# Kernel optimization log

Measured on AMD Instinct MI355X. Metric: run time of the kernel, lower is better.

Reference implementation:

```python
import jax, jax.numpy as jnp
import numpy as np

B, TQ, TV, D, UNITS = 4, 256, 256, 512, 512
NEG_INF = -1e9

def setup_inputs() -> dict:
    key = jax.random.key(0)
    ks = jax.random.split(key, 5)
    return {
        "query": jax.random.normal(ks[0], (B, TQ, D), dtype=jnp.float32),
        "value": jax.random.normal(ks[1], (B, TV, D), dtype=jnp.float32),
        "mask": jnp.ones((B, TV), dtype=bool),
        "W1": jax.random.normal(ks[2], (D, UNITS), dtype=jnp.float32) * (1.0 / np.sqrt(D)),
        "W2": jax.random.normal(ks[3], (D, UNITS), dtype=jnp.float32) * (1.0 / np.sqrt(D)),
        "scale": jax.random.normal(ks[4], (UNITS,), dtype=jnp.float32),
    }

def reference(query, value, mask, W1, W2, scale):
    # Dual projections
    q = query @ W1                      # [B,Tq,U]
    k = value @ W2                      # [B,Tv,U]
    # Additive (Bahdanau) scores: sum(scale * tanh(q + k)) over units
    # broadcast tensor [B,Tq,Tv,U] is what the kernel would tile/fuse away
    t = jnp.tanh(q[:, :, None, :] + k[:, None, :, :])   # [B,Tq,Tv,U]
    scores = jnp.einsum('btvu,u->btv', t, scale)         # [B,Tq,Tv]
    # mask over value (key) positions
    scores = jnp.where(mask[:, None, :], scores, NEG_INF)
    attn = jax.nn.softmax(scores, axis=-1)               # [B,Tq,Tv]
    context = jnp.einsum('btv,bvd->btd', attn, value)    # [B,Tq,D]
    return context, attn
```

## Files before the change

### kernel.cpp

```cpp
#include <hip/hip_runtime.h>

typedef float f4 __attribute__((ext_vector_type(4)));
typedef float f2 __attribute__((ext_vector_type(2)));
typedef short short8 __attribute__((ext_vector_type(8)));
typedef float f32x4 __attribute__((ext_vector_type(4)));

#define NEG_INF -1e9f

__device__ inline void bsplit(float x, unsigned short& h, unsigned short& l) {
  union { float f; unsigned u; } a; a.f = x;
  unsigned rh = (a.u + 0x7fffu + ((a.u >> 16) & 1u)) >> 16;
  h = (unsigned short)rh;
  union { unsigned u; float f; } b; b.u = rh << 16;
  union { float f; unsigned u; } c; c.f = x - b.f;
  unsigned rl = (c.u + 0x7fffu + ((c.u >> 16) & 1u)) >> 16;
  l = (unsigned short)rl;
}

__device__ inline void gl_lds16(const void* g, void* l) {
  __builtin_amdgcn_global_load_lds(
      (const __attribute__((address_space(1))) unsigned int*)g,
      (__attribute__((address_space(3))) unsigned int*)l, 16, 0, 0);
}

__global__ __launch_bounds__(256) void conv_aw(
    const float* __restrict__ q, const float* __restrict__ v,
    const float* __restrict__ W1, const float* __restrict__ W2,
    unsigned short* __restrict__ Ahi, unsigned short* __restrict__ Alo,
    unsigned short* __restrict__ Whi, unsigned short* __restrict__ Wlo)
{
  __shared__ float ldsW[128][64];
  const int t = threadIdx.x;

  if (blockIdx.x < 512) {
    const int g = blockIdx.x * 256 + t;
    const int row64 = g & 63;
    const int panel = (g >> 6) & 31;
    const int kc    = g >> 11;
    const int rowg  = panel * 64 + row64;
    const float* src = (rowg < 1024) ? (q + (size_t)rowg * 512 + kc * 8)
                                     : (v + (size_t)(rowg - 1024) * 512 + kc * 8);
    f4 x0 = *reinterpret_cast<const f4*>(src);
    f4 x1 = *reinterpret_cast<const f4*>(src + 4);
    unsigned short h[8], l[8];
#pragma unroll
    for (int j = 0; j < 4; ++j) { bsplit(x0[j], h[j], l[j]); bsplit(x1[j], h[4+j], l[4+j]); }
    const size_t off = ((size_t)(panel * 64 + kc) * 64 + row64) * 8;
    short8 ph, pl;
#pragma unroll
    for (int j = 0; j < 8; ++j) { ph[j] = (short)h[j]; pl[j] = (short)l[j]; }
    *reinterpret_cast<short8*>(&Ahi[off]) = ph;
    *reinterpret_cast<short8*>(&Alo[off]) = pl;
    return;
  }

  const int bid   = blockIdx.x - 512;
  const int kslab = bid & 3;
  const int np    = (bid >> 2) & 7;
  const int z     = bid >> 5;
  const float* __restrict__ W = z ? W2 : W1;
  const int k0 = kslab * 128, n0 = np * 64;

#pragma unroll
  for (int it = 0; it < 8; ++it) {
    const int idx = it * 256 + t;
    const int kr  = idx >> 4;
    const int nc4 = (idx & 15) * 4;
    *reinterpret_cast<f4*>(&ldsW[kr][nc4]) =
        *reinterpret_cast<const f4*>(&W[(size_t)(k0 + kr) * 512 + n0 + nc4]);
  }
  __syncthreads();

  const int wpanel = z * 8 + np;
  const int n = t & 63;
#pragma unroll
  for (int it = 0; it < 4; ++it) {
    const int kcl = it * 4 + (t >> 6);
    short8 ph, pl;
#pragma unroll
    for (int j = 0; j < 8; ++j) {
      unsigned short h, l;
      bsplit(ldsW[kcl * 8 + j][n], h, l);
      ph[j] = (short)h; pl[j] = (short)l;
    }
    const size_t off = ((size_t)(wpanel * 64 + kslab * 16 + kcl) * 64 + n) * 8;
    *reinterpret_cast<short8*>(&Whi[off]) = ph;
    *reinterpret_cast<short8*>(&Wlo[off]) = pl;
  }
}

__global__ __launch_bounds__(256) void projmm(
    const unsigned short* __restrict__ Ahi, const unsigned short* __restrict__ Alo,
    const unsigned short* __restrict__ Whi, const unsigned short* __restrict__ Wlo,
    float* __restrict__ EQ, float* __restrict__ EKT)
{
  const int nb = blockIdx.x, mb = blockIdx.y, z = blockIdx.z;
  const int t = threadIdx.x;
  const int l = t & 63;
  const int w = t >> 6;
  const int wr = w >> 1, wc = w & 1;

  __shared__ __align__(16) short Ast[2][2][2048];
  __shared__ __align__(16) short Bst[2][2][2048];
  __shared__ float ldsT[64][67];

  const unsigned short* abase_h = Ahi + (size_t)(z * 16 + mb) * 32768;
  const unsigned short* abase_l = Alo + (size_t)(z * 16 + mb) * 32768;
  const unsigned short* wbase_h = Whi + (size_t)(z * 8 + nb) * 32768;
  const unsigned short* wbase_l = Wlo + (size_t)(z * 8 + nb) * 32768;

  const int ldst = (t >> 6) * 512;
  const int gsrc = t * 8;

#define STAGE(buf, ks)                                                        \
  do {                                                                        \
    gl_lds16(abase_h + (ks) * 2048 + gsrc, &Ast[buf][0][ldst]);               \
    gl_lds16(abase_l + (ks) * 2048 + gsrc, &Ast[buf][1][ldst]);               \
    gl_lds16(wbase_h + (ks) * 2048 + gsrc, &Bst[buf][0][ldst]);               \
    gl_lds16(wbase_l + (ks) * 2048 + gsrc, &Bst[buf][1][ldst]);               \
  } while (0)

  f32x4 acc[2][2] = {};
  STAGE(0, 0);
  __syncthreads();

  int buf = 0;
  for (int ks = 0; ks < 16; ++ks) {
    if (ks < 15) STAGE(buf ^ 1, ks + 1);
    const int kgo = (l >> 4) * 1024;
    short8 ah[2], al[2], bh[2], bl[2];
#pragma unroll
    for (int i = 0; i < 2; ++i) {
      const int ro = (wr * 32 + i * 16 + (l & 15)) * 16;
      ah[i] = *reinterpret_cast<const short8*>((const char*)&Ast[buf][0][0] + kgo + ro);
      al[i] = *reinterpret_cast<const short8*>((const char*)&Ast[buf][1][0] + kgo + ro);
    }
#pragma unroll
    for (int j = 0; j < 2; ++j) {
      const int co = (wc * 32 + j * 16 + (l & 15)) * 16;
      bh[j] = *reinterpret_cast<const short8*>((const char*)&Bst[buf][0][0] + kgo + co);
      bl[j] = *reinterpret_cast<const short8*>((const char*)&Bst[buf][1][0] + kgo + co);
    }
#pragma unroll
    for (int i = 0; i < 2; ++i)
#pragma unroll
      for (int j = 0; j < 2; ++j) {
        acc[i][j] = __builtin_amdgcn_mfma_f32_16x16x32_bf16(ah[i], bh[j], acc[i][j], 0, 0, 0);
        acc[i][j] = __builtin_amdgcn_mfma_f32_16x16x32_bf16(ah[i], bl[j], acc[i][j], 0, 0, 0);
        acc[i][j] = __builtin_amdgcn_mfma_f32_16x16x32_bf16(al[i], bh[j], acc[i][j], 0, 0, 0);
      }
    __syncthreads();
    buf ^= 1;
  }

  if (z == 0) {
#pragma unroll
    for (int i = 0; i < 2; ++i)
#pragma unroll
      for (int j = 0; j < 2; ++j)
#pragma unroll
        for (int r = 0; r < 4; ++r) {
          const int row = mb * 64 + wr * 32 + i * 16 + (l >> 4) * 4 + r;
          const int col = nb * 64 + wc * 32 + j * 16 + (l & 15);
          EQ[(size_t)row * 512 + col] = __expf(2.0f * acc[i][j][r]);
        }
  } else {
#pragma unroll
    for (int i = 0; i < 2; ++i)
#pragma unroll
      for (int j = 0; j < 2; ++j)
#pragma unroll
        for (int r = 0; r < 4; ++r) {
          const int rl = wr * 32 + i * 16 + (l >> 4) * 4 + r;
          const int cl = wc * 32 + j * 16 + (l & 15);
          ldsT[rl][cl] = __expf(2.0f * acc[i][j][r]);
        }
    __syncthreads();
    const int b  = (mb * 64) >> 8;
    const int v0 = (mb * 64) & 255;
    const int vl = t & 63;
#pragma unroll
    for (int it = 0; it < 16; ++it) {
      const int ul = it * 4 + (t >> 6);
      EKT[(size_t)b * 131072 + (size_t)(nb * 64 + ul) * 256 + v0 + vl] = ldsT[vl][ul];
    }
  }
#undef STAGE
}

__global__ __launch_bounds__(1024) void bah_attn(
    const float* __restrict__ EQ, const float* __restrict__ EKT,
    const float* __restrict__ value, const int* __restrict__ mask,
    const float* __restrict__ scale,
    float* __restrict__ ctx_out, float* __restrict__ attn_out)
{
  const int blk = blockIdx.x;
  const int b  = (blk & 7) >> 1;
  const int tg = (blk >> 3) + ((blk & 1) << 5);
  const int tq0 = tg * 4;
  const int bq  = b * 256 + tq0;

  const int tid = threadIdx.x;
  const int v4  = tid & 63;
  const int uq  = tid >> 6;
  const int w   = tid >> 6;
  const int l   = tid & 63;

  __shared__ f4    eq4s[512];
  __shared__ float ss[512];
  __shared__ float wredM[4][4];
  __shared__ float wredS[4][4];
  __shared__ float sumS_lds;
  __shared__ float atT[256][4];
  __shared__ __align__(16) char uA[131072];
  float* const ubufF = (float*)uA;
  float* const partF = (float*)uA;
  float* const ctxpF = (float*)(uA + 65536);

  const float* __restrict__ ekb = EKT + (size_t)b * (512 * 256);
  const float* __restrict__ eqb = EQ + (size_t)bq * 512;

  const int u0 = uq * 32;
  float* const wbase = ubufF + uq * 2048;

#define STAGEW(bufp, s)                                                       \
  do {                                                                        \
    _Pragma("unroll")                                                         \
    for (int c_ = 0; c_ < 4; ++c_)                                            \
      gl_lds16(ekb + (size_t)(u0 + (s) * 4 + c_) * 256 + l * 4,               \
               wbase + (bufp) * 1024 + c_ * 256);                             \
  } while (0)

  STAGEW(0, 0);

  if (tid < 512) {
    f4 e;
    e[0] = eqb[tid];
    e[1] = eqb[512 + tid];
    e[2] = eqb[1024 + tid];
    e[3] = eqb[1536 + tid];
    eq4s[tid] = e;
    ss[tid] = scale[tid];
  }
  __syncthreads();

  if (w == 0) {
    float s = 0.f;
#pragma unroll
    for (int j = 0; j < 8; ++j) s += ss[l + 64 * j];
#pragma unroll
    for (int off = 32; off; off >>= 1) s += __shfl_xor(s, off);
    if (l == 0) sumS_lds = s;
  }

  f2 accp[4][2] = {};
  int bufi = 0;
#pragma unroll 1
  for (int s = 0; s < 8; ++s) {
    if (s < 7) {
      STAGEW(bufi ^ 1, s + 1);
      asm volatile("s_waitcnt vmcnt(4)" ::: "memory");
    } else {
      asm volatile("s_waitcnt vmcnt(0)" ::: "memory");
    }
    __builtin_amdgcn_sched_barrier(0);
    const float* bp = wbase + bufi * 1024;
#pragma unroll
    for (int cp = 0; cp < 2; ++cp) {
      const int uA_ = u0 + s * 4 + 2 * cp;
      const f4 ekA4 = *reinterpret_cast<const f4*>(bp + (2 * cp) * 256 + v4 * 4);
      const f4 ekB4 = *reinterpret_cast<const f4*>(bp + (2 * cp + 1) * 256 + v4 * 4);
      const f2 ekA[2] = {{ekA4[0], ekA4[1]}, {ekA4[2], ekA4[3]}};
      const f2 ekB[2] = {{ekB4[0], ekB4[1]}, {ekB4[2], ekB4[3]}};
      const f4 eqA = eq4s[uA_];
      const f4 eqB = eq4s[uA_ + 1];
      const f2 sp  = *reinterpret_cast<const f2*>(&ss[uA_]);
      const f2 sA2 = {sp[0], sp[0]};
      const f2 sB2 = {sp[1], sp[1]};
      const f2 one2 = {1.0f, 1.0f};
#pragma unroll
      for (int i = 0; i < 4; ++i) {
        const f2 eA2 = {eqA[i], eqA[i]};
        const f2 eB2 = {eqB[i], eqB[i]};
#pragma unroll
        for (int jh = 0; jh < 2; ++jh) {
          const f2 dA  = __builtin_elementwise_fma(eA2, ekA[jh], one2);
          const f2 dB  = __builtin_elementwise_fma(eB2, ekB[jh], one2);
          const f2 num = __builtin_elementwise_fma(sA2, dB, sB2 * dA);
          const f2 P   = dA * dB;
          f2 r;
          r[0] = __builtin_amdgcn_rcpf(P[0]);
          r[1] = __builtin_amdgcn_rcpf(P[1]);
          accp[i][jh] = __builtin_elementwise_fma(num, r, accp[i][jh]);
        }
      }
    }
    bufi ^= 1;
  }

  __syncthreads();
#pragma unroll
  for (int i = 0; i < 4; ++i) {
    const f4 a4 = {accp[i][0][0], accp[i][0][1], accp[i][1][0], accp[i][1][1]};
    *reinterpret_cast<f4*>(partF + uq * 1024 + i * 256 + v4 * 4) = a4;
  }
  __syncthreads();

  const int r   = w & 3;
  const int vg  = w >> 2;
  const int v   = vg * 64 + l;
  float sc, ex;
  {
    float p = 0.f;
#pragma unroll
    for (int u2 = 0; u2 < 16; ++u2) p += partF[u2 * 1024 + r * 256 + v];
    const bool mok = (mask[b * 256 + v] != 0);
    sc = mok ? (sumS_lds - 2.0f * p) : NEG_INF;
    float m = sc;
#pragma unroll
    for (int off = 32; off; off >>= 1) m = fmaxf(m, __shfl_xor(m, off));
    if (l == 0) wredM[r][vg] = m;
  }
  __syncthreads();

  {
    const float m = fmaxf(fmaxf(wredM[r][0], wredM[r][1]),
                          fmaxf(wredM[r][2], wredM[r][3]));
    ex = __expf(sc - m);
    float sm = ex;
#pragma unroll
    for (int off = 32; off; off >>= 1) sm += __shfl_xor(sm, off);
    if (l == 0) wredS[r][vg] = sm;
  }
  __syncthreads();

  {
    const float denom = (wredS[r][0] + wredS[r][1]) + (wredS[r][2] + wredS[r][3]);
    const float a = ex * __builtin_amdgcn_rcpf(denom);
    atT[v][r] = a;
    attn_out[(size_t)(bq + r) * 256 + v] = a;
  }
  __syncthreads();

  const int vc8 = w & 7;
  const int dh  = w >> 3;
  const float* __restrict__ vb = value + (size_t)b * (256 * 512) + dh * 256;
  f4 c0 = {0,0,0,0}, c1 = {0,0,0,0}, c2 = {0,0,0,0}, c3 = {0,0,0,0};
#pragma unroll 4
  for (int v2 = 0; v2 < 32; ++v2) {
    const int vv = vc8 * 32 + v2;
    const f4 a4 = *reinterpret_cast<const f4*>(&atT[vv][0]);
    const f4 x  = *reinterpret_cast<const f4*>(&vb[(size_t)vv * 512 + l * 4]);
    c0 += a4[0] * x;
    c1 += a4[1] * x;
    c2 += a4[2] * x;
    c3 += a4[3] * x;
  }
  {
    float* const cp = ctxpF + vc8 * 2048 + dh * 256 + l * 4;
    *reinterpret_cast<f4*>(cp + 0 * 512) = c0;
    *reinterpret_cast<f4*>(cp + 1 * 512) = c1;
    *reinterpret_cast<f4*>(cp + 2 * 512) = c2;
    *reinterpret_cast<f4*>(cp + 3 * 512) = c3;
  }
  __syncthreads();

  {
    const int row = tid >> 8;
    const int d2  = (tid & 255) * 2;
    f2 s = {0.f, 0.f};
#pragma unroll
    for (int vc = 0; vc < 8; ++vc)
      s += *reinterpret_cast<const f2*>(ctxpF + vc * 2048 + row * 512 + d2);
    *reinterpret_cast<f2*>(&ctx_out[(size_t)(bq + row) * 512 + d2]) = s;
  }
#undef STAGEW
}

extern "C" void kernel_launch(void* const* d_in, const int* in_sizes, int n_in,
                              void* d_out, int out_size, void* d_ws, size_t ws_size,
                              hipStream_t stream) {
  const float* query = (const float*)d_in[0];
  const float* value = (const float*)d_in[1];
  const int*   mask  = (const int*)d_in[2];
  const float* W1    = (const float*)d_in[3];
  const float* W2    = (const float*)d_in[4];
  const float* scale = (const float*)d_in[5];

  char* ws = (char*)d_ws;
  float* EQ  = (float*)(ws);
  float* EKT = (float*)(ws + (2u << 20));
  unsigned short* Ahi = (unsigned short*)(ws + (4u << 20));
  unsigned short* Alo = (unsigned short*)(ws + (6u << 20));
  unsigned short* Whi = (unsigned short*)(ws + (8u << 20));
  unsigned short* Wlo = (unsigned short*)(ws + (9u << 20));

  float* ctx  = (float*)d_out;
  float* attn = ctx + 4 * 256 * 512;

  conv_aw<<<dim3(576), 256, 0, stream>>>(query, value, W1, W2, Ahi, Alo, Whi, Wlo);
  projmm<<<dim3(8, 16, 2), 256, 0, stream>>>(Ahi, Alo, Whi, Wlo, EQ, EKT);
  bah_attn<<<dim3(256), 1024, 0, stream>>>(EQ, EKT, value, mask, scale, ctx, attn);
}
```

Measured before the change: 46.78 us.

## Split context matmul out of attention kernel into separate tiled GEMM

```diff
diff --git a/kernel.cpp b/kernel.cpp
--- a/kernel.cpp
+++ b/kernel.cpp
@@ -190,9 +190,8 @@
 
 __global__ __launch_bounds__(1024) void bah_attn(
     const float* __restrict__ EQ, const float* __restrict__ EKT,
-    const float* __restrict__ value, const int* __restrict__ mask,
-    const float* __restrict__ scale,
-    float* __restrict__ ctx_out, float* __restrict__ attn_out)
+    const int* __restrict__ mask, const float* __restrict__ scale,
+    float* __restrict__ attn_out)
 {
   const int blk = blockIdx.x;
   const int b  = (blk & 7) >> 1;
@@ -211,11 +210,9 @@
   __shared__ float wredM[4][4];
   __shared__ float wredS[4][4];
   __shared__ float sumS_lds;
-  __shared__ float atT[256][4];
   __shared__ __align__(16) char uA[131072];
   float* const ubufF = (float*)uA;
   float* const partF = (float*)uA;
-  float* const ctxpF = (float*)(uA + 65536);
 
   const float* __restrict__ ekb = EKT + (size_t)b * (512 * 256);
   const float* __restrict__ eqb = EQ + (size_t)bq * 512;
@@ -337,44 +334,68 @@
   {
     const float denom = (wredS[r][0] + wredS[r][1]) + (wredS[r][2] + wredS[r][3]);
     const float a = ex * __builtin_amdgcn_rcpf(denom);
-    atT[v][r] = a;
     attn_out[(size_t)(bq + r) * 256 + v] = a;
   }
-  __syncthreads();
-
-  const int vc8 = w & 7;
-  const int dh  = w >> 3;
-  const float* __restrict__ vb = value + (size_t)b * (256 * 512) + dh * 256;
-  f4 c0 = {0,0,0,0}, c1 = {0,0,0,0}, c2 = {0,0,0,0}, c3 = {0,0,0,0};
-#pragma unroll 4
-  for (int v2 = 0; v2 < 32; ++v2) {
-    const int vv = vc8 * 32 + v2;
-    const f4 a4 = *reinterpret_cast<const f4*>(&atT[vv][0]);
-    const f4 x  = *reinterpret_cast<const f4*>(&vb[(size_t)vv * 512 + l * 4]);
-    c0 += a4[0] * x;
-    c1 += a4[1] * x;
-    c2 += a4[2] * x;
-    c3 += a4[3] * x;
-  }
-  {
-    float* const cp = ctxpF + vc8 * 2048 + dh * 256 + l * 4;
-    *reinterpret_cast<f4*>(cp + 0 * 512) = c0;
-    *reinterpret_cast<f4*>(cp + 1 * 512) = c1;
-    *reinterpret_cast<f4*>(cp + 2 * 512) = c2;
-    *reinterpret_cast<f4*>(cp + 3 * 512) = c3;
-  }
-  __syncthreads();
-
-  {
-    const int row = tid >> 8;
-    const int d2  = (tid & 255) * 2;
-    f2 s = {0.f, 0.f};
-#pragma unroll
-    for (int vc = 0; vc < 8; ++vc)
-      s += *reinterpret_cast<const f2*>(ctxpF + vc * 2048 + row * 512 + d2);
-    *reinterpret_cast<f2*>(&ctx_out[(size_t)(bq + row) * 512 + d2]) = s;
-  }
 #undef STAGEW
+}
+
+__global__ __launch_bounds__(256) void ctxmm(
+    const float* __restrict__ attn, const float* __restrict__ value,
+    float* __restrict__ ctx)
+{
+  const int nt = blockIdx.x;
+  const int mt = blockIdx.y;
+  const int b  = blockIdx.z;
+  const int tq0 = mt * 64, d0 = nt * 64;
+
+  const float* __restrict__ A = attn + (size_t)b * 65536;
+  const float* __restrict__ B = value + (size_t)b * 131072;
+
+  __shared__ float As[32][68];
+  __shared__ float Bs[32][68];
+
+  const int t = threadIdx.x;
+  const int tx = t & 15;
+  const int ty = t >> 4;
+
+  float acc[4][4] = {};
+
+  for (int kb = 0; kb < 256; kb += 32) {
+#pragma unroll
+    for (int t2 = 0; t2 < 2; ++t2) {
+      const int id  = t2 * 256 + t;
+      const int ar  = id >> 3;
+      const int akc = (id & 7) * 4;
+      f4 av = *reinterpret_cast<const f4*>(&A[(size_t)(tq0 + ar) * 256 + kb + akc]);
+      As[akc + 0][ar] = av[0];
+      As[akc + 1][ar] = av[1];
+      As[akc + 2][ar] = av[2];
+      As[akc + 3][ar] = av[3];
+      const int bk = id >> 4;
+      const int bc = (id & 15) * 4;
+      *reinterpret_cast<f4*>(&Bs[bk][bc]) =
+          *reinterpret_cast<const f4*>(&B[(size_t)(kb + bk) * 512 + d0 + bc]);
+    }
+    __syncthreads();
+#pragma unroll
+    for (int kk = 0; kk < 32; ++kk) {
+      f4 a  = *reinterpret_cast<const f4*>(&As[kk][ty * 4]);
+      f4 bb = *reinterpret_cast<const f4*>(&Bs[kk][tx * 4]);
+#pragma unroll
+      for (int i = 0; i < 4; ++i)
+#pragma unroll
+        for (int j = 0; j < 4; ++j)
+          acc[i][j] = fmaf(a[i], bb[j], acc[i][j]);
+    }
+    __syncthreads();
+  }
+
+#pragma unroll
+  for (int i = 0; i < 4; ++i) {
+    f4 r = {acc[i][0], acc[i][1], acc[i][2], acc[i][3]};
+    *reinterpret_cast<f4*>(
+        &ctx[(size_t)b * 131072 + (size_t)(tq0 + ty * 4 + i) * 512 + d0 + tx * 4]) = r;
+  }
 }
 
 extern "C" void kernel_launch(void* const* d_in, const int* in_sizes, int n_in,
@@ -400,5 +421,6 @@
 
   conv_aw<<<dim3(576), 256, 0, stream>>>(query, value, W1, W2, Ahi, Alo, Whi, Wlo);
   projmm<<<dim3(8, 16, 2), 256, 0, stream>>>(Ahi, Alo, Whi, Wlo, EQ, EKT);
-  bah_attn<<<dim3(256), 1024, 0, stream>>>(EQ, EKT, value, mask, scale, ctx, attn);
-}
+  bah_attn<<<dim3(256), 1024, 0, stream>>>(EQ, EKT, mask, scale, attn);
+  ctxmm<<<dim3(8, 4, 4), 256, 0, stream>>>(attn, value, ctx);
+}
```

After: 53.69 us. +14.8%, slower.
